# Kernel optimization log

Measured on AMD Instinct MI355X. Metric: run time of the kernel, lower is better.

Reference implementation:

```python
import jax, jax.numpy as jnp
import numpy as np

N_QUBITS = 12
N_LAYERS = 6
BATCH = 2048
N_OUTPUTS = 2
C64 = jnp.complex64


def setup_inputs() -> dict:
    key = jax.random.key(0)
    k1, k2 = jax.random.split(key)
    x = jax.random.normal(k1, (BATCH, N_QUBITS), dtype=jnp.float32)
    # nn.Parameter: torch.randn(n_layers, n_qubits, 3) * 0.1
    weights = jax.random.normal(k2, (N_LAYERS, N_QUBITS, 3), dtype=jnp.float32) * 0.1
    return {"x": x, "weights": weights}


def _rx(t):
    # t: (...,) angles -> (..., 2, 2) RX matrices
    c = jnp.cos(t * 0.5).astype(C64)
    s = (-1j * jnp.sin(t * 0.5)).astype(C64)
    return jnp.stack([jnp.stack([c, s], -1), jnp.stack([s, c], -1)], -2)


def _ry(t):
    c = jnp.cos(t * 0.5).astype(C64)
    s = jnp.sin(t * 0.5).astype(C64)
    return jnp.stack([jnp.stack([c, -s], -1), jnp.stack([s, c], -1)], -2)


def _rz(t):
    e = jnp.exp(-0.5j * t).astype(C64)
    z = jnp.zeros_like(e)
    return jnp.stack([jnp.stack([e, z], -1), jnp.stack([z, jnp.conj(e)], -1)], -2)


def _rot(w):
    # PennyLane Rot(phi, theta, omega) = RZ(omega) @ RY(theta) @ RZ(phi); w: (n_qubits, 3)
    return _rz(w[:, 2]) @ _ry(w[:, 1]) @ _rz(w[:, 0])


def _apply_1q(state, gate, q):
    # state: (B, 2**n) complex; gate: (2,2) or (B,2,2); qubit q (wire 0 = MSB)
    B = state.shape[0]
    s = state.reshape(B, 2 ** q, 2, -1)
    if gate.ndim == 3:
        s = jnp.einsum('bij,bljr->blir', gate, s)
    else:
        s = jnp.einsum('ij,bljr->blir', gate, s)
    return s.reshape(B, -1)


def _apply_cnot(state, c, t, n):
    # control c, target t; flip target axis where control bit == 1
    B = state.shape[0]
    s = state.reshape((B,) + (2,) * n)
    ac, at = 1 + c, 1 + t
    s0 = jnp.take(s, 0, axis=ac)
    s1 = jnp.take(s, 1, axis=ac)
    at2 = at - 1 if at > ac else at
    s1 = jnp.flip(s1, axis=at2)
    s = jnp.stack([s0, s1], axis=ac)
    return s.reshape(B, -1)


def _layer(state, w, n):
    # strongly-entangling layer: Rot on every wire, then full CNOT entanglement
    rot = _rot(w)  # (n, 2, 2)
    for q in range(n):
        state = _apply_1q(state, rot[q], q)
    for i in range(n):
        for j in range(i + 1, n):
            state = _apply_cnot(state, i, j, n)
    return state


def _forward(x, weights):
    n = N_QUBITS
    B = x.shape[0]
    state = jnp.zeros((B, 2 ** n), C64).at[:, 0].set(1.0)
    # angle encoding: RX(x_q) on wire q (PennyLane AngleEmbedding default axis X)
    for q in range(n):
        state = _apply_1q(state, _rx(x[:, q]), q)
    layer_ckpt = jax.checkpoint(lambda s, w: _layer(s, w, n))
    for l in range(N_LAYERS):
        state = layer_ckpt(state, weights[l])
    # expval(PauliZ) on wires 0..n_outputs-1
    probs = state.real ** 2 + state.imag ** 2  # (B, 2**n)
    outs = []
    for k in range(N_OUTPUTS):
        p = probs.reshape(B, 2 ** k, 2, -1)
        outs.append(p[:, :, 0, :].sum((1, 2)) - p[:, :, 1, :].sum((1, 2)))
    return jnp.stack(outs, -1)  # (B, n_outputs)


def reference(x, weights):
    return _forward(x, weights)
```

## Files before the change

kernel.cpp:

```cpp
#include <hip/hip_runtime.h>
#include <math.h>

#define NQ 12
#define DIM 4096
#define NL 6
#define TPB 256

typedef float f2 __attribute__((ext_vector_type(2)));


__device__ __forceinline__ f2 pk_mul(f2 a, f2 b) {
  f2 d; asm("v_pk_mul_f32 %0, %1, %2" : "=v"(d) : "v"(a), "v"(b)); return d;
}
__device__ __forceinline__ f2 pk_fma(f2 a, f2 b, f2 c) {
  f2 d; asm("v_pk_fma_f32 %0, %1, %2, %3" : "=v"(d) : "v"(a), "v"(b), "v"(c)); return d;
}
__device__ __forceinline__ f2 cmulp(f2 a, f2 c) {
  f2 r1, d;
  asm("v_pk_mul_f32 %0, %1, %2 op_sel:[0,0] op_sel_hi:[0,1]"
      : "=v"(r1) : "v"(a), "v"(c));
  asm("v_pk_fma_f32 %0, %1, %2, %3 op_sel:[1,1,0] op_sel_hi:[1,0,1] neg_lo:[1,0,0]"
      : "=v"(d) : "v"(a), "v"(c), "v"(r1));
  return d;
}

template<int BIT>
__device__ __forceinline__ void apply_ry16(f2 v[16], f2 cc, f2 ss) {
  #pragma unroll
  for (int j = 0; j < 16; ++j) {
    if (j & (1 << BIT)) continue;
    const int k = j | (1 << BIT);
    f2 a = v[j], b = v[k];
    f2 t1 = pk_mul(a, cc);
    f2 t2 = pk_mul(a, ss);
    f2 na; asm("v_pk_fma_f32 %0, %1, %2, %3 neg_lo:[1,0,0] neg_hi:[1,0,0]"
               : "=v"(na) : "v"(b), "v"(ss), "v"(t1));
    f2 nb = pk_fma(b, cc, t2);
    v[j] = na; v[k] = nb;
  }
}

__global__ __launch_bounds__(TPB, 4)
void qsim12_kernel(const float* __restrict__ x, const float* __restrict__ w,
                   float* __restrict__ out) {
  __shared__ __align__(16) float st[2*DIM];
  __shared__ __align__(16) float4 ryt[NL*NQ];
  __shared__ f2 zA[NL*16];
  __shared__ f2 zC[NL*16];
  __shared__ f2 phw[NL*NQ];
  __shared__ float2 cs[NQ];

  const int t = threadIdx.x;
  const int b = blockIdx.x;
  char* stb = (char*)st;

  if (t < 96) {
    int l = t >> 4, j = t & 15;
    float ph = 0.f;
    #pragma unroll
    for (int m = 0; m < 4; ++m) {
      float phi = w[(l*NQ + (11 - m))*3 + 0];
      ph += ((j >> m) & 1) ? phi : -phi;
    }
    float sv, cv; sincosf(0.5f*ph, &sv, &cv);
    zA[t] = (f2){cv, sv};
  } else if (t < 192) {
    int g = t - 96, l = g >> 4, j = g & 15;
    float ph = 0.f;
    #pragma unroll
    for (int m = 0; m < 4; ++m) {
      float om = w[(l*NQ + (3 - m))*3 + 2];
      ph += ((j >> m) & 1) ? om : -om;
    }
    float sv, cv; sincosf(0.5f*ph, &sv, &cv);
    zC[g] = (f2){cv, sv};
  } else {
    int g = t - 192;
    float th = w[g*3 + 1];
    float sv, cv; sincosf(0.5f*th, &sv, &cv);
    ryt[g] = make_float4(cv, cv, sv, sv);
    phw[g] = (f2){w[g*3 + 0], w[g*3 + 2]};
  }
  if (t < 8) {
    int g = 64 + t;
    float th = w[g*3 + 1];
    float sv, cv; sincosf(0.5f*th, &sv, &cv);
    ryt[g] = make_float4(cv, cv, sv, sv);
    phw[g] = (f2){w[g*3 + 0], w[g*3 + 2]};
  }
  if (t >= 244) {
    int q = t - 244;
    float xv = x[b*NQ + q];
    float sv, cv; sincosf(0.5f*xv, &sv, &cv);
    cs[q] = make_float2(cv, sv);
  }
  __syncthreads();

  int baseA[8], baseB[8];
  #pragma unroll
  for (int m = 0; m < 8; ++m) {
    baseA[m] = (t << 7) + (((2*m) ^ (t & 14)) << 3);
    baseB[m] = ((t >> 4) << 11) + ((((t & 15) ^ (2*m))) << 3);
  }
  const int baseC = ((t >> 4) << 7) + ((((t & 15) ^ ((t >> 4) & 15))) << 3);
  const int G = t ^ (t >> 1);
  int baseS[2];
  #pragma unroll
  for (int par = 0; par < 2; ++par) {
    const int k8 = par << 3;
    baseS[par] = ((((G >> 4) & 15) ^ k8) << 7)
               + ((((G & 15) ^ ((G >> 4) & 14) ^ k8)) << 3);
  }
  float sg[8];
  #pragma unroll
  for (int k = 0; k < 8; ++k) sg[k] = ((t >> k) & 1) ? 0.5f : -0.5f;

  f2 v[16];

  {
    float2 csr[NQ];
    #pragma unroll
    for (int q = 0; q < NQ; ++q) csr[q] = cs[q];
    float rhi = 1.f;
    #pragma unroll
    for (int k = 0; k < 8; ++k)
      rhi *= ((t >> k) & 1) ? csr[7-k].y : csr[7-k].x;
    const int popt = __popc(t);
    #pragma unroll
    for (int j = 0; j < 16; ++j) {
      float r = rhi;
      #pragma unroll
      for (int m = 0; m < 4; ++m)
        r *= ((j >> m) & 1) ? csr[11-m].y : csr[11-m].x;
      const int pj = (popt + __popc(j)) & 3;
      if      (pj == 0) v[j] = (f2){ r, 0.f};
      else if (pj == 1) v[j] = (f2){0.f, -r};
      else if (pj == 2) v[j] = (f2){-r, 0.f};
      else              v[j] = (f2){0.f,  r};
    }
  }

  #define RY(BIT, WQ)                                               \
    { float4 r = ryt[l*NQ + (WQ)];                                  \
      apply_ry16<BIT>(v, (f2){r.x, r.y}, (f2){r.z, r.w}); }

  #pragma unroll 1
  for (int l = 0; l < NL; ++l) {
    float fa = 0.f, fc = 0.f;
    #pragma unroll
    for (int k = 0; k < 8; ++k) {
      fa += sg[k] * phw[l*NQ + 7 - k].x;
      fc += sg[k] * phw[l*NQ + 11 - k].y;
    }
    f2 wA, wC;
    { float sv, cv; sincosf(fa, &sv, &cv); wA = (f2){cv, sv};
      sincosf(fc, &sv, &cv); wC = (f2){cv, sv}; }

    if (l > 0) {
      #pragma unroll
      for (int m = 0; m < 8; ++m) {
        float4 q4 = *(const float4*)(stb + baseA[m]);
        v[2*m]   = (f2){q4.x, q4.y};
        v[2*m+1] = (f2){q4.z, q4.w};
      }
    }
    #pragma unroll
    for (int j = 0; j < 16; ++j) {
      f2 z = zA[l*16 + j];
      v[j] = cmulp(cmulp(v[j], z), wA);
    }
    RY(0,11) RY(1,10) RY(2,9) RY(3,8)
    #pragma unroll
    for (int m = 0; m < 8; ++m)
      *(float4*)(stb + baseA[m]) =
          make_float4(v[2*m].x, v[2*m].y, v[2*m+1].x, v[2*m+1].y);
    __syncthreads();

    #pragma unroll
    for (int m = 0; m < 8; ++m) {
      v[2*m]   = *(const f2*)(stb + baseB[m] + (2*m)*128);
      v[2*m+1] = *(const f2*)(stb + baseB[m] + (2*m+1)*128);
    }
    RY(0,7) RY(1,6) RY(2,5) RY(3,4)
    #pragma unroll
    for (int m = 0; m < 8; ++m) {
      *(f2*)(stb + baseB[m] + (2*m)*128)         = v[2*m];
      *(f2*)(stb + (baseB[m] ^ 8) + (2*m+1)*128) = v[2*m+1];
    }
    __syncthreads();

    #pragma unroll
    for (int j = 0; j < 16; ++j)
      v[j] = *(const f2*)(stb + baseC + j*2048);
    RY(0,3) RY(1,2) RY(2,1) RY(3,0)
    if (l < NL-1) {
      #pragma unroll
      for (int j = 0; j < 16; ++j) {
        f2 z = zC[l*16 + j];
        v[j] = cmulp(cmulp(v[j], z), wC);
      }
      #pragma unroll
      for (int j = 0; j < 16; ++j) {
        const int g4 = (j ^ (j >> 1)) & 15;
        *(f2*)(stb + baseS[j & 1] + (g4 << 11)) = v[j];
      }
      __syncthreads();
    }
  }

  float a0 = 0.f, a1 = 0.f;
  #pragma unroll
  for (int j = 0; j < 16; ++j) {
    float pr = v[j].x*v[j].x + v[j].y*v[j].y;
    a0 += ((j >> 3) & 1) ? -pr : pr;
    a1 += (((j >> 2) ^ (j >> 3)) & 1) ? -pr : pr;
  }
  #pragma unroll
  for (int off = 32; off >= 1; off >>= 1) {
    a0 += __shfl_down(a0, off);
    a1 += __shfl_down(a1, off);
  }
  __syncthreads();
  if ((t & 63) == 0) { st[(t >> 6)*2] = a0; st[(t >> 6)*2 + 1] = a1; }
  __syncthreads();
  if (t == 0) {
    out[b*2 + 0] = st[0] + st[2] + st[4] + st[6];
    out[b*2 + 1] = st[1] + st[3] + st[5] + st[7];
  }
}

extern "C" void kernel_launch(void* const* d_in, const int* in_sizes, int n_in,
                              void* d_out, int out_size, void* d_ws, size_t ws_size,
                              hipStream_t stream) {
  const float* x = (const float*)d_in[0];
  const float* w = (const float*)d_in[1];
  float* out = (float*)d_out;
  int B = in_sizes[0] / NQ;
  qsim12_kernel<<<B, TPB, 0, stream>>>(x, w, out);
}
```

Before: 136.7 us.

## Precompute weight-only phase tables in a prep kernel and fuse RZ phases across layers

A single-block prep kernel now computes all weight-dependent phase factors and RY cos/sin tables into workspace memory. The trailing RZ(omega) of layer l and the leading RZ(phi) of layer l+1 are merged into one phase multiply, which the CNOT permutation makes possible via Gray-code indexing. The per-block shared-memory setup, its barrier and the per-layer sincosf calls are removed. Input angles are now spread with readlane instead of going through shared memory, and the occupancy hint rises from 4 to 5 blocks. The cost is a second kernel launch and reading the tables from global memory or cache.

```diff
diff --git a/kernel.cpp b/kernel.cpp
--- a/kernel.cpp
+++ b/kernel.cpp
@@ -6,8 +6,15 @@
 #define NL 6
 #define TPB 256
 
+
+#define WS_WA0 0
+#define WS_W   512
+#define WS_ZA0 3072
+#define WS_ZM  3104
+#define WS_RYT 3424
+#define WS_FLOATS 3712
+
 typedef float f2 __attribute__((ext_vector_type(2)));
-
 
 __device__ __forceinline__ f2 pk_mul(f2 a, f2 b) {
   f2 d; asm("v_pk_mul_f32 %0, %1, %2" : "=v"(d) : "v"(a), "v"(b)); return d;
@@ -40,61 +47,98 @@
   }
 }
 
-__global__ __launch_bounds__(TPB, 4)
-void qsim12_kernel(const float* __restrict__ x, const float* __restrict__ w,
+__global__ __launch_bounds__(256)
+void qprep_kernel(const float* __restrict__ w, float* __restrict__ ws) {
+  const int t = threadIdx.x;
+
+  {
+    float f = 0.f;
+    #pragma unroll
+    for (int k = 0; k < 8; ++k) {
+      float p = w[(0*NQ + 7 - k)*3 + 0];
+      f += ((t >> k) & 1) ? 0.5f*p : -0.5f*p;
+    }
+    float sv, cv; sincosf(f, &sv, &cv);
+    ws[WS_WA0 + 2*t] = cv; ws[WS_WA0 + 2*t + 1] = sv;
+  }
+
+  #pragma unroll 1
+  for (int l = 0; l < NL-1; ++l) {
+    float f = 0.f;
+    const int gt = t ^ (t >> 1);
+    #pragma unroll
+    for (int k = 0; k < 8; ++k) {
+      float om = w[(l*NQ + 11 - k)*3 + 2];
+      f += ((t >> k) & 1) ? 0.5f*om : -0.5f*om;
+    }
+    #pragma unroll
+    for (int k = 0; k < 7; ++k) {
+      float ph = w[((l+1)*NQ + 11 - k)*3 + 0];
+      f += ((gt >> k) & 1) ? 0.5f*ph : -0.5f*ph;
+    }
+    float sv, cv; sincosf(f, &sv, &cv);
+    ws[WS_W + (l*256 + t)*2] = cv; ws[WS_W + (l*256 + t)*2 + 1] = sv;
+  }
+
+  if (t < 16) {
+    float f = 0.f;
+    #pragma unroll
+    for (int m = 0; m < 4; ++m) {
+      float p = w[(0*NQ + 11 - m)*3 + 0];
+      f += ((t >> m) & 1) ? 0.5f*p : -0.5f*p;
+    }
+    float sv, cv; sincosf(f, &sv, &cv);
+    ws[WS_ZA0 + 2*t] = cv; ws[WS_ZA0 + 2*t + 1] = sv;
+  }
+
+  if (t < 160) {
+    const int l = t >> 5, h = (t >> 4) & 1, j = t & 15;
+    float f = 0.f;
+    #pragma unroll
+    for (int m = 0; m < 4; ++m) {
+      float om = w[(l*NQ + 3 - m)*3 + 2];
+      f += ((j >> m) & 1) ? 0.5f*om : -0.5f*om;
+    }
+    {
+      float p4 = w[((l+1)*NQ + 4)*3 + 0];
+      f += (h ^ (j & 1)) ? 0.5f*p4 : -0.5f*p4;
+    }
+    const int gj = j ^ (j >> 1);
+    #pragma unroll
+    for (int m = 0; m < 4; ++m) {
+      float ph = w[((l+1)*NQ + 3 - m)*3 + 0];
+      f += ((gj >> m) & 1) ? 0.5f*ph : -0.5f*ph;
+    }
+    float sv, cv; sincosf(f, &sv, &cv);
+    ws[WS_ZM + 2*t] = cv; ws[WS_ZM + 2*t + 1] = sv;
+  }
+
+  if (t < 72) {
+    float sv, cv; sincosf(0.5f*w[t*3 + 1], &sv, &cv);
+    ((float4*)(ws + WS_RYT))[t] = make_float4(cv, cv, sv, sv);
+  }
+}
+
+__global__ __launch_bounds__(TPB, 5)
+void qsim12_kernel(const float* __restrict__ x, const float* __restrict__ ws,
                    float* __restrict__ out) {
   __shared__ __align__(16) float st[2*DIM];
-  __shared__ __align__(16) float4 ryt[NL*NQ];
-  __shared__ f2 zA[NL*16];
-  __shared__ f2 zC[NL*16];
-  __shared__ f2 phw[NL*NQ];
-  __shared__ float2 cs[NQ];
 
   const int t = threadIdx.x;
   const int b = blockIdx.x;
   char* stb = (char*)st;
 
-  if (t < 96) {
-    int l = t >> 4, j = t & 15;
-    float ph = 0.f;
-    #pragma unroll
-    for (int m = 0; m < 4; ++m) {
-      float phi = w[(l*NQ + (11 - m))*3 + 0];
-      ph += ((j >> m) & 1) ? phi : -phi;
-    }
-    float sv, cv; sincosf(0.5f*ph, &sv, &cv);
-    zA[t] = (f2){cv, sv};
-  } else if (t < 192) {
-    int g = t - 96, l = g >> 4, j = g & 15;
-    float ph = 0.f;
-    #pragma unroll
-    for (int m = 0; m < 4; ++m) {
-      float om = w[(l*NQ + (3 - m))*3 + 2];
-      ph += ((j >> m) & 1) ? om : -om;
-    }
-    float sv, cv; sincosf(0.5f*ph, &sv, &cv);
-    zC[g] = (f2){cv, sv};
-  } else {
-    int g = t - 192;
-    float th = w[g*3 + 1];
-    float sv, cv; sincosf(0.5f*th, &sv, &cv);
-    ryt[g] = make_float4(cv, cv, sv, sv);
-    phw[g] = (f2){w[g*3 + 0], w[g*3 + 2]};
-  }
-  if (t < 8) {
-    int g = 64 + t;
-    float th = w[g*3 + 1];
-    float sv, cv; sincosf(0.5f*th, &sv, &cv);
-    ryt[g] = make_float4(cv, cv, sv, sv);
-    phw[g] = (f2){w[g*3 + 0], w[g*3 + 2]};
-  }
-  if (t >= 244) {
-    int q = t - 244;
-    float xv = x[b*NQ + q];
+  float csx[NQ], csy[NQ];
+  {
+    const int q = t & 63;
+    float xv = (q < NQ) ? x[b*NQ + q] : 0.f;
     float sv, cv; sincosf(0.5f*xv, &sv, &cv);
-    cs[q] = make_float2(cv, sv);
-  }
-  __syncthreads();
+    #pragma unroll
+    for (int qq = 0; qq < NQ; ++qq) {
+      csx[qq] = __int_as_float(__builtin_amdgcn_readlane(__float_as_int(cv), qq));
+      csy[qq] = __int_as_float(__builtin_amdgcn_readlane(__float_as_int(sv), qq));
+    }
+  }
 
   int baseA[8], baseB[8];
   #pragma unroll
@@ -111,27 +155,21 @@
     baseS[par] = ((((G >> 4) & 15) ^ k8) << 7)
                + ((((G & 15) ^ ((G >> 4) & 14) ^ k8)) << 3);
   }
-  float sg[8];
-  #pragma unroll
-  for (int k = 0; k < 8; ++k) sg[k] = ((t >> k) & 1) ? 0.5f : -0.5f;
 
   f2 v[16];
 
   {
-    float2 csr[NQ];
-    #pragma unroll
-    for (int q = 0; q < NQ; ++q) csr[q] = cs[q];
     float rhi = 1.f;
     #pragma unroll
     for (int k = 0; k < 8; ++k)
-      rhi *= ((t >> k) & 1) ? csr[7-k].y : csr[7-k].x;
+      rhi *= ((t >> k) & 1) ? csy[7-k] : csx[7-k];
     const int popt = __popc(t);
     #pragma unroll
     for (int j = 0; j < 16; ++j) {
       float r = rhi;
       #pragma unroll
       for (int m = 0; m < 4; ++m)
-        r *= ((j >> m) & 1) ? csr[11-m].y : csr[11-m].x;
+        r *= ((j >> m) & 1) ? csy[11-m] : csx[11-m];
       const int pj = (popt + __popc(j)) & 3;
       if      (pj == 0) v[j] = (f2){ r, 0.f};
       else if (pj == 1) v[j] = (f2){0.f, -r};
@@ -140,22 +178,12 @@
     }
   }
 
-  #define RY(BIT, WQ)                                               \
-    { float4 r = ryt[l*NQ + (WQ)];                                  \
+  #define RY(BIT, WQ)                                                     \
+    { const float4 r = *(const float4*)(ws + WS_RYT + 4*(l*NQ + (WQ)));   \
       apply_ry16<BIT>(v, (f2){r.x, r.y}, (f2){r.z, r.w}); }
 
   #pragma unroll 1
   for (int l = 0; l < NL; ++l) {
-    float fa = 0.f, fc = 0.f;
-    #pragma unroll
-    for (int k = 0; k < 8; ++k) {
-      fa += sg[k] * phw[l*NQ + 7 - k].x;
-      fc += sg[k] * phw[l*NQ + 11 - k].y;
-    }
-    f2 wA, wC;
-    { float sv, cv; sincosf(fa, &sv, &cv); wA = (f2){cv, sv};
-      sincosf(fc, &sv, &cv); wC = (f2){cv, sv}; }
-
     if (l > 0) {
       #pragma unroll
       for (int m = 0; m < 8; ++m) {
@@ -163,11 +191,14 @@
         v[2*m]   = (f2){q4.x, q4.y};
         v[2*m+1] = (f2){q4.z, q4.w};
       }
-    }
-    #pragma unroll
-    for (int j = 0; j < 16; ++j) {
-      f2 z = zA[l*16 + j];
-      v[j] = cmulp(cmulp(v[j], z), wA);
+    } else {
+      const float2 wv = *(const float2*)(ws + WS_WA0 + 2*t);
+      const f2 wA0 = (f2){wv.x, wv.y};
+      #pragma unroll
+      for (int j = 0; j < 16; ++j) {
+        const float2 zv = *(const float2*)(ws + WS_ZA0 + 2*j);
+        v[j] = cmulp(cmulp(v[j], (f2){zv.x, zv.y}), wA0);
+      }
     }
     RY(0,11) RY(1,10) RY(2,9) RY(3,8)
     #pragma unroll
@@ -194,10 +225,13 @@
       v[j] = *(const f2*)(stb + baseC + j*2048);
     RY(0,3) RY(1,2) RY(2,1) RY(3,0)
     if (l < NL-1) {
+      const float2 wv = *(const float2*)(ws + WS_W + (l*TPB + t)*2);
+      const f2 W = (f2){wv.x, wv.y};
+      const float* zmb = ws + WS_ZM + ((l*2 + ((t >> 7) & 1))*16)*2;
       #pragma unroll
       for (int j = 0; j < 16; ++j) {
-        f2 z = zC[l*16 + j];
-        v[j] = cmulp(cmulp(v[j], z), wC);
+        const float2 zv = *(const float2*)(zmb + 2*j);
+        v[j] = cmulp(cmulp(v[j], (f2){zv.x, zv.y}), W);
       }
       #pragma unroll
       for (int j = 0; j < 16; ++j) {
@@ -235,6 +269,8 @@
   const float* x = (const float*)d_in[0];
   const float* w = (const float*)d_in[1];
   float* out = (float*)d_out;
+  float* ws = (float*)d_ws;
   int B = in_sizes[0] / NQ;
-  qsim12_kernel<<<B, TPB, 0, stream>>>(x, w, out);
-}
+  qprep_kernel<<<1, 256, 0, stream>>>(w, ws);
+  qsim12_kernel<<<B, TPB, 0, stream>>>(x, ws, out);
+}
```

Result: faster. 128.9 us (-5.7%).
